# Optimization experiments

Measured on AMD Instinct MI355X. Metric: run time of the kernel, lower is better.

Reference implementation:

```python
import jax, jax.numpy as jnp
import numpy as np

N_USER = 50000
N_ITEM = 30000
NNZ = 500000  # user-item interactions; edges duplicated symmetrically -> E = 2*NNZ
EMB = 64
N_LAYERS = 2
N_FACTORS = 4
N_ITERATIONS = 2


def setup_inputs() -> dict:
    key = jax.random.key(0)
    k1, k2, k3, k4 = jax.random.split(key, 4)
    user_emb = jax.random.normal(k1, (N_USER, EMB), dtype=jnp.float32) * 0.1
    item_emb = jax.random.normal(k2, (N_ITEM, EMB), dtype=jnp.float32) * 0.1
    row = jax.random.randint(k3, (NNZ,), 0, N_USER, dtype=jnp.int32)
    col = jax.random.randint(k4, (NNZ,), 0, N_ITEM, dtype=jnp.int32) + N_USER
    # symmetric edge list exactly as the torch module builds it
    all_h_list = jnp.concatenate([row, col], axis=0)
    all_t_list = jnp.concatenate([col, row], axis=0)
    return {"user_emb": user_emb, "item_emb": item_emb,
            "all_h_list": all_h_list, "all_t_list": all_t_list}


def _dgcf_forward(user_emb, item_emb, all_h_list, all_t_list):
    n_user = user_emb.shape[0]
    ego = jnp.concatenate([user_emb, item_emb], axis=0)  # [N, D]
    N, D = ego.shape
    F = N_FACTORS
    d = D // F
    E = all_h_list.shape[0]
    dtype = ego.dtype

    all_embeddings = [ego]
    A = jnp.ones((E, F), dtype=dtype)  # A_values init

    for _layer in range(N_LAYERS):
        # torch.chunk along dim 1 == reshape [N, F, d]
        chunks = ego.reshape(N, F, d)
        tail_chunks = chunks[all_t_list]  # [E, F, d] gather of tail embeddings
        factor_emb = None
        for _t in range(N_ITERATIONS):
            # build_matrix, vectorized over the F factors
            normA = jax.nn.softmax(A, axis=1)                        # [E, F]
            dval = jax.ops.segment_sum(normA, all_h_list, num_segments=N)  # [N, F]
            dinv = 1.0 / jnp.sqrt(jnp.clip(dval, 1e-8))
            edge_weight = normA * dinv[all_h_list] * dinv[all_t_list]  # [E, F]
            # message passing per factor: gather tail, weight, scatter to head
            edge_val = tail_chunks * edge_weight[:, :, None]           # [E, F, d]
            factor_emb = jax.ops.segment_sum(edge_val, all_h_list, num_segments=N)  # [N, F, d]
            # dynamic routing update of A
            head = factor_emb[all_h_list]                              # [E, F, d]
            head = head / jnp.clip(jnp.linalg.norm(head, axis=-1, keepdims=True), 1e-12)
            tail = tail_chunks / jnp.clip(jnp.linalg.norm(tail_chunks, axis=-1, keepdims=True), 1e-12)
            A_iter = jnp.sum(head * jnp.tanh(tail), axis=-1)           # [E, F]
            A = A + A_iter
        ego = factor_emb.reshape(N, D)  # concat of factor chunks (last iteration)
        all_embeddings.append(ego)

    all_emb = jnp.mean(jnp.stack(all_embeddings, axis=1), axis=1)  # [N, D]
    return all_emb[:n_user], all_emb[n_user:]


def reference(user_emb, item_emb, all_h_list, all_t_list):
    return _dgcf_forward(user_emb, item_emb, all_h_list, all_t_list)
```

## Files before the change

kernel.cpp:

```cpp
#include <hip/hip_runtime.h>
#include <hip/hip_bf16.h>

#define N_USER 50000
#define N_ITEM 30000
#define NTOT   80000
#define EMB    64
#define FAC    4
#define EDGES  1000000
#define LOG4   1.3862943611198906f
#define NBUCK  512
#define BBLK   512
#define BCH    1954


__device__ inline float bf2f(unsigned short u) {
    return __uint_as_float(((unsigned int)u) << 16);
}
__device__ inline unsigned short f2bf(float f) {
    unsigned int x = __float_as_uint(f);
    x += 0x7FFFu + ((x >> 16) & 1u);
    return (unsigned short)(x >> 16);
}
__device__ inline float dot2(unsigned int a, unsigned int b) {
    float a0 = __uint_as_float(a << 16), a1 = __uint_as_float(a & 0xFFFF0000u);
    float b0 = __uint_as_float(b << 16), b1 = __uint_as_float(b & 0xFFFF0000u);
    return a0 * b0 + a1 * b1;
}
__device__ inline int bucket_of(int h) { return (int)(((unsigned)h * NBUCK) / (unsigned)NTOT); }
__device__ inline int bucket_lo(int k) { return (k * NTOT + NBUCK - 1) / NBUCK; }

__global__ void k_detect(const unsigned short* __restrict__ raw, int* __restrict__ flag) {
    __shared__ int s;
    if (threadIdx.x == 0) s = 0;
    __syncthreads();
    int c = 0;
    for (int i = threadIdx.x; i < 16384; i += 256) {
        unsigned short u = raw[i];
        if ((u & 0x7F80) == 0x7F80) c++;
    }
    atomicAdd(&s, c);
    __syncthreads();
    if (threadIdx.x == 0) *flag = (s > 0) ? 1 : 0;
}

__global__ void k_init(const void* __restrict__ ue, const void* __restrict__ ie,
                       const int* __restrict__ flag,
                       unsigned short* __restrict__ egoh,
                       unsigned short* __restrict__ tnh0) {
    int gid = blockIdx.x * blockDim.x + threadIdx.x;
    int wid = gid >> 6;
    int lane = threadIdx.x & 63;
    if (wid >= NTOT) return;
    int i = wid * 64 + lane;
    bool isf32 = (*flag != 0);
    float v;
    if (i < N_USER * EMB) {
        v = isf32 ? ((const float*)ue)[i]
                  : __bfloat162float(((const __hip_bfloat16*)ue)[i]);
    } else {
        int j = i - N_USER * EMB;
        v = isf32 ? ((const float*)ie)[j]
                  : __bfloat162float(((const __hip_bfloat16*)ie)[j]);
    }
    egoh[i] = f2bf(v);
    float ss = v * v;
    ss += __shfl_xor(ss, 1); ss += __shfl_xor(ss, 2);
    ss += __shfl_xor(ss, 4); ss += __shfl_xor(ss, 8);
    float rr = 1.0f / fmaxf(sqrtf(ss), 1e-12f);
    tnh0[i] = f2bf(tanhf(v * rr));
}

__global__ void k_bcnt(const int* __restrict__ hl, int* __restrict__ cnt) {
    __shared__ int hist[NBUCK];
    int b = blockIdx.x, tid = threadIdx.x;
    for (int i = tid; i < NBUCK; i += 256) hist[i] = 0;
    __syncthreads();
    int base = b * BCH, end = base + BCH; if (end > EDGES) end = EDGES;
    for (int e = base + tid; e < end; e += 256)
        atomicAdd(&hist[bucket_of(hl[e])], 1);
    __syncthreads();
    for (int i = tid; i < NBUCK; i += 256) cnt[b * NBUCK + i] = hist[i];
}

__global__ void k_btot(const int* __restrict__ cnt, int* __restrict__ boff) {
    __shared__ int sbuf[NBUCK];
    int k = threadIdx.x;
    int s = 0;
    for (int b = 0; b < BBLK; ++b) s += cnt[b * NBUCK + k];
    sbuf[k] = s;
    __syncthreads();
    int v = s;
    for (int st = 1; st < NBUCK; st <<= 1) {
        int t = (k >= st) ? sbuf[k - st] : 0;
        __syncthreads();
        sbuf[k] += t;
        __syncthreads();
    }
    boff[k] = sbuf[k] - v;
    if (k == NBUCK - 1) boff[NBUCK] = EDGES;
}

__global__ void k_bscan(const int* __restrict__ cnt, const int* __restrict__ boff,
                        int* __restrict__ gbase) {
    __shared__ int buf[BBLK];
    int k = blockIdx.x, tid = threadIdx.x;
    int v = cnt[tid * NBUCK + k];
    buf[tid] = v;
    __syncthreads();
    for (int s = 1; s < BBLK; s <<= 1) {
        int t = (tid >= s) ? buf[tid - s] : 0;
        __syncthreads();
        buf[tid] += t;
        __syncthreads();
    }
    gbase[tid * NBUCK + k] = boff[k] + buf[tid] - v;
}

__global__ void k_bscat(const int* __restrict__ hl, const int* __restrict__ tl,
                        const int* __restrict__ gbase, int* __restrict__ bt) {
    __shared__ int lg[NBUCK];
    int b = blockIdx.x, tid = threadIdx.x;
    for (int i = tid; i < NBUCK; i += 256) lg[i] = gbase[b * NBUCK + i];
    __syncthreads();
    int base = b * BCH, end = base + BCH; if (end > EDGES) end = EDGES;
    for (int e = base + tid; e < end; e += 256) {
        int h = hl[e];
        int k = bucket_of(h);
        int pos = atomicAdd(&lg[k], 1);
        bt[pos] = ((h - bucket_lo(k)) << 17) | tl[e];
    }
}

__global__ void k_bfin(const int* __restrict__ bt, const int* __restrict__ boff,
                       int* __restrict__ off, float* __restrict__ dvacc,
                       int* __restrict__ tlist, int* __restrict__ hlist) {
    __shared__ int ldeg[160];
    __shared__ int lcur[160];
    __shared__ int sbuf[256];
    int k = blockIdx.x, tid = threadIdx.x;
    int lo = bucket_lo(k), hi = bucket_lo(k + 1);
    int nn = hi - lo;
    for (int i = tid; i < nn; i += 256) ldeg[i] = 0;
    __syncthreads();
    int start = boff[k], end = boff[k + 1];
    for (int j = start + tid; j < end; j += 256)
        atomicAdd(&ldeg[bt[j] >> 17], 1);
    __syncthreads();
    int v = (tid < nn) ? ldeg[tid] : 0;
    sbuf[tid] = v;
    __syncthreads();
    for (int s = 1; s < 256; s <<= 1) {
        int t = (tid >= s) ? sbuf[tid - s] : 0;
        __syncthreads();
        sbuf[tid] += t;
        __syncthreads();
    }
    if (tid < nn) {
        int o = start + sbuf[tid] - v;
        off[lo + tid] = o;
        lcur[tid] = o;
        float d = 0.25f * (float)v;
        ((float4*)dvacc)[lo + tid] = make_float4(d, d, d, d);
    }
    if (k == 0 && tid == 0) off[NTOT] = EDGES;
    __syncthreads();
    for (int j = start + tid; j < end; j += 256) {
        int val = bt[j];
        int hrel = val >> 17;
        int t = val & 0x1FFFF;
        int pos = atomicAdd(&lcur[hrel], 1);
        tlist[pos] = t;
        hlist[pos] = lo + hrel;
    }
}

__global__ void k_scale(float* __restrict__ dvacc, float* __restrict__ dvinv,
                        const unsigned short* __restrict__ ego,
                        unsigned short* __restrict__ egoS) {
    int gid = blockIdx.x * blockDim.x + threadIdx.x;
    int wid = gid >> 6;
    int lane = threadIdx.x & 63;
    if (wid >= NTOT) return;
    int f = lane >> 4;
    float r = rsqrtf(fmaxf(dvacc[wid * 4 + f], 1e-8f));
    if ((lane & 15) == 0) dvinv[wid * 4 + f] = r;
    if (lane < 4) dvacc[wid * 4 + lane] = 0.f;
    int i = wid * 64 + lane;
    egoS[i] = f2bf(bf2f(ego[i]) * r);
}

__global__ void k_mp(const unsigned short* __restrict__ egoS, const float* __restrict__ P,
                     const float* __restrict__ dvinv, const int* __restrict__ off,
                     const int* __restrict__ tlist,
                     unsigned short* __restrict__ fach, float* __restrict__ rhn,
                     unsigned short* __restrict__ tnhOut,
                     int useP, int writeRhn, int writeTnh) {
    int gid = blockIdx.x * blockDim.x + threadIdx.x;
    int wid = gid >> 6;
    int lane = threadIdx.x & 63;
    if (wid >= NTOT) return;
    int c = lane & 15;
    int q = lane >> 4;
    int f = c >> 2;
    int beg = off[wid], end = off[wid + 1];
    float dvh = dvinv[wid * 4 + f];
    const uint2* eg2 = (const uint2*)egoS;

    float a0 = 0.f, a1 = 0.f, a2 = 0.f, a3 = 0.f;
    int nfull = (end - beg) >> 2;
    int j = beg + q;
    if (useP) {
#pragma unroll 2
        for (int g = 0; g < nfull; ++g, j += 4) {
            int t = tlist[j];
            float w = P[j * 4 + f];
            uint2 u = eg2[t * 16 + c];
            a0 += w * __uint_as_float(u.x << 16);
            a1 += w * __uint_as_float(u.x & 0xFFFF0000u);
            a2 += w * __uint_as_float(u.y << 16);
            a3 += w * __uint_as_float(u.y & 0xFFFF0000u);
        }
        if (j < end) {
            int t = tlist[j];
            float w = P[j * 4 + f];
            uint2 u = eg2[t * 16 + c];
            a0 += w * __uint_as_float(u.x << 16);
            a1 += w * __uint_as_float(u.x & 0xFFFF0000u);
            a2 += w * __uint_as_float(u.y << 16);
            a3 += w * __uint_as_float(u.y & 0xFFFF0000u);
        }
    } else {
#pragma unroll 2
        for (int g = 0; g < nfull; ++g, j += 4) {
            int t = tlist[j];
            uint2 u = eg2[t * 16 + c];
            a0 += __uint_as_float(u.x << 16);
            a1 += __uint_as_float(u.x & 0xFFFF0000u);
            a2 += __uint_as_float(u.y << 16);
            a3 += __uint_as_float(u.y & 0xFFFF0000u);
        }
        if (j < end) {
            int t = tlist[j];
            uint2 u = eg2[t * 16 + c];
            a0 += __uint_as_float(u.x << 16);
            a1 += __uint_as_float(u.x & 0xFFFF0000u);
            a2 += __uint_as_float(u.y << 16);
            a3 += __uint_as_float(u.y & 0xFFFF0000u);
        }
        a0 *= 0.25f; a1 *= 0.25f; a2 *= 0.25f; a3 *= 0.25f;
    }

    a0 += __shfl_xor(a0, 16); a1 += __shfl_xor(a1, 16);
    a2 += __shfl_xor(a2, 16); a3 += __shfl_xor(a3, 16);
    a0 += __shfl_xor(a0, 32); a1 += __shfl_xor(a1, 32);
    a2 += __shfl_xor(a2, 32); a3 += __shfl_xor(a3, 32);

    a0 *= dvh; a1 *= dvh; a2 *= dvh; a3 *= dvh;

    if (q == 0) {
        unsigned int p01 = (unsigned int)f2bf(a0) | ((unsigned int)f2bf(a1) << 16);
        unsigned int p23 = (unsigned int)f2bf(a2) | ((unsigned int)f2bf(a3) << 16);
        ((uint2*)fach)[wid * 16 + c] = make_uint2(p01, p23);
    }

    if (writeRhn || writeTnh) {
        float ss = a0 * a0 + a1 * a1 + a2 * a2 + a3 * a3;
        ss += __shfl_xor(ss, 1); ss += __shfl_xor(ss, 2);
        float rr = 1.0f / fmaxf(sqrtf(ss), 1e-12f);
        if (writeRhn && q == 0 && (c & 3) == 0) rhn[wid * 4 + f] = rr;
        if (writeTnh) {
            float t0 = tanhf(a0 * rr), t1 = tanhf(a1 * rr),
                  t2 = tanhf(a2 * rr), t3 = tanhf(a3 * rr);
            if (q == 0) {
                unsigned int p01 = (unsigned int)f2bf(t0) | ((unsigned int)f2bf(t1) << 16);
                unsigned int p23 = (unsigned int)f2bf(t2) | ((unsigned int)f2bf(t3) << 16);
                ((uint2*)tnhOut)[wid * 16 + c] = make_uint2(p01, p23);
            }
        }
    }
}

__global__ void k_upd(const unsigned short* __restrict__ fach,
                      const unsigned short* __restrict__ tnhh,
                      const float* __restrict__ rhn,
                      const int* __restrict__ hlist, const int* __restrict__ tlist,
                      float* __restrict__ P, float* __restrict__ dval, int first) {
    __shared__ int   s_h[256];
    __shared__ float s_p[256][4];
    int tid = threadIdx.x;
    int j = blockIdx.x * 256 + tid;
    int h = -1;
    if (j < EDGES) {
        h = hlist[j];
        int t = tlist[j];
        const uint4* frow = (const uint4*)(fach + (size_t)h * 64);
        const uint4* trow = (const uint4*)(tnhh + (size_t)t * 64);
        float d[4];
#pragma unroll
        for (int f = 0; f < 4; ++f) {
            uint4 a0 = frow[f * 2], a1 = frow[f * 2 + 1];
            uint4 b0 = trow[f * 2], b1 = trow[f * 2 + 1];
            d[f] = dot2(a0.x, b0.x) + dot2(a0.y, b0.y)
                 + dot2(a0.z, b0.z) + dot2(a0.w, b0.w)
                 + dot2(a1.x, b1.x) + dot2(a1.y, b1.y)
                 + dot2(a1.z, b1.z) + dot2(a1.w, b1.w);
        }
        float4 rh = ((const float4*)rhn)[h];
        float lx, ly, lz, lw;
        if (first) { lx = ly = lz = lw = -LOG4; }
        else {
            float4 p0 = ((const float4*)P)[j];
            lx = __logf(p0.x); ly = __logf(p0.y);
            lz = __logf(p0.z); lw = __logf(p0.w);
        }
        float y0 = lx + rh.x * d[0], y1 = ly + rh.y * d[1],
              y2 = lz + rh.z * d[2], y3 = lw + rh.w * d[3];
        float m = fmaxf(fmaxf(y0, y1), fmaxf(y2, y3));
        float e0 = __expf(y0 - m), e1 = __expf(y1 - m),
              e2 = __expf(y2 - m), e3 = __expf(y3 - m);
        float inv = 1.0f / (e0 + e1 + e2 + e3);
        float p0n = e0 * inv, p1n = e1 * inv, p2n = e2 * inv, p3n = e3 * inv;
        ((float4*)P)[j] = make_float4(p0n, p1n, p2n, p3n);
        s_p[tid][0] = p0n; s_p[tid][1] = p1n; s_p[tid][2] = p2n; s_p[tid][3] = p3n;
    }
    s_h[tid] = h;
    __syncthreads();
    if (h == -1) return;
    if (tid > 0 && s_h[tid - 1] == h) return;
    float a0 = 0.f, a1 = 0.f, a2 = 0.f, a3 = 0.f;
    int k = tid;
    while (k < 256 && s_h[k] == h) {
        a0 += s_p[k][0]; a1 += s_p[k][1]; a2 += s_p[k][2]; a3 += s_p[k][3];
        ++k;
    }
    float* dst = dval + (size_t)h * 4;
    if (tid == 0 || k == 256) {
        unsafeAtomicAdd(dst + 0, a0);
        unsafeAtomicAdd(dst + 1, a1);
        unsafeAtomicAdd(dst + 2, a2);
        unsafeAtomicAdd(dst + 3, a3);
    } else {
        ((float4*)dst)[0] = make_float4(a0, a1, a2, a3);
    }
}

__global__ void k_final(const void* __restrict__ ue, const void* __restrict__ ie,
                        const int* __restrict__ flag,
                        const unsigned short* __restrict__ f1,
                        const unsigned short* __restrict__ f3,
                        float* __restrict__ out) {
    int i = blockIdx.x * blockDim.x + threadIdx.x;
    if (i >= NTOT * EMB) return;
    bool isf32 = (*flag != 0);
    float v;
    if (i < N_USER * EMB) {
        v = isf32 ? ((const float*)ue)[i]
                  : __bfloat162float(((const __hip_bfloat16*)ue)[i]);
    } else {
        int j = i - N_USER * EMB;
        v = isf32 ? ((const float*)ie)[j]
                  : __bfloat162float(((const __hip_bfloat16*)ie)[j]);
    }
    out[i] = (v + bf2f(f1[i]) + bf2f(f3[i])) * (1.0f / 3.0f);
}

extern "C" void kernel_launch(void* const* d_in, const int* in_sizes, int n_in,
                              void* d_out, int out_size, void* d_ws, size_t ws_size,
                              hipStream_t stream) {
    const void* ue = d_in[0];
    const void* ie = d_in[1];
    const int* hl = (const int*)d_in[2];
    const int* tl = (const int*)d_in[3];
    float* out = (float*)d_out;

    float* ws    = (float*)d_ws;
    float* P     = ws;
    int*   bt    = (int*)(ws);
    int*   cnt   = (int*)(ws + 1000000);
    int*   gbase = (int*)(ws + 1262144);
    float* dvacc = ws + 4000000;
    float* dvinv = ws + 4320000;
    float* rhn   = ws + 4640000;
    unsigned short* bufW = (unsigned short*)(ws + 4960000);
    unsigned short* bufX = (unsigned short*)(ws + 7520000);
    unsigned short* bufY = (unsigned short*)(ws + 10080000);
    unsigned short* bufZ0 = (unsigned short*)(ws + 12640000);
    unsigned short* bufZ1 = (unsigned short*)(ws + 15200000);
    unsigned short* egoS = (unsigned short*)(ws + 17760000);
    int*   flag = (int*)(ws + 20320000);
    int*   boff = (int*)(ws + 20320016);
    int*   off  = (int*)(ws + 20400016);
    int*   tlist = (int*)(ws + 20480017);
    int*   hlist = (int*)(ws + 21480017);

    k_detect<<<1, 256, 0, stream>>>((const unsigned short*)ue, flag);
    k_init<<<20000, 256, 0, stream>>>(ue, ie, flag, bufW, bufZ0);

    k_bcnt<<<BBLK, 256, 0, stream>>>(hl, cnt);
    k_btot<<<1, NBUCK, 0, stream>>>(cnt, boff);
    k_bscan<<<NBUCK, BBLK, 0, stream>>>(cnt, boff, gbase);
    k_bscat<<<BBLK, 256, 0, stream>>>(hl, tl, gbase, bt);
    k_bfin<<<NBUCK, 256, 0, stream>>>(bt, boff, off, dvacc, tlist, hlist);

    k_scale<<<20000, 256, 0, stream>>>(dvacc, dvinv, bufW, egoS);
    k_mp<<<20000, 256, 0, stream>>>(egoS, P, dvinv, off, tlist, bufX, rhn, bufZ1,
                                    0, 1, 0);
    k_upd<<<3907, 256, 0, stream>>>(bufX, bufZ0, rhn, hlist, tlist, P, dvacc, 1);
    k_scale<<<20000, 256, 0, stream>>>(dvacc, dvinv, bufW, egoS);
    k_mp<<<20000, 256, 0, stream>>>(egoS, P, dvinv, off, tlist, bufY, rhn, bufZ1,
                                    1, 1, 1);
    k_upd<<<3907, 256, 0, stream>>>(bufY, bufZ0, rhn, hlist, tlist, P, dvacc, 0);
    k_scale<<<20000, 256, 0, stream>>>(dvacc, dvinv, bufY, egoS);
    k_mp<<<20000, 256, 0, stream>>>(egoS, P, dvinv, off, tlist, bufX, rhn, bufZ1,
                                    1, 1, 0);
    k_upd<<<3907, 256, 0, stream>>>(bufX, bufZ1, rhn, hlist, tlist, P, dvacc, 0);
    k_scale<<<20000, 256, 0, stream>>>(dvacc, dvinv, bufY, egoS);
    k_mp<<<20000, 256, 0, stream>>>(egoS, P, dvinv, off, tlist, bufW, rhn, bufZ1,
                                    1, 0, 0);
    k_final<<<20000, 256, 0, stream>>>(ue, ie, flag, bufY, bufW, out);
}
```

Baseline: 441.1 us.

## Fuse routing-update pass into the CSR message-passing kernel

Folds the per-edge routing/softmax update (previously a separate edge-parallel kernel reading the head-factor embedding, a norm buffer and an hlist array) into the node-wise CSR message-passing kernel. Each wavefront keeps its just-computed head factor and norm in registers, re-walks its neighbour list to compute dot products with tail tanh embeddings, updates P, and writes the degree sums directly without atomics. This removes a kernel launch, the hlist array, the rhn buffer and the atomic degree accumulation. In exchange, the second neighbour walk runs inside the lane-serial CSR loop with extra shuffles, and the per-edge P accesses become strided scalar loads.

Result: slower. 484.1 us (+9.7%).

```diff
diff --git a/kernel.cpp b/kernel.cpp
--- a/kernel.cpp
+++ b/kernel.cpp
@@ -20,11 +20,6 @@
     unsigned int x = __float_as_uint(f);
     x += 0x7FFFu + ((x >> 16) & 1u);
     return (unsigned short)(x >> 16);
-}
-__device__ inline float dot2(unsigned int a, unsigned int b) {
-    float a0 = __uint_as_float(a << 16), a1 = __uint_as_float(a & 0xFFFF0000u);
-    float b0 = __uint_as_float(b << 16), b1 = __uint_as_float(b & 0xFFFF0000u);
-    return a0 * b0 + a1 * b1;
 }
 __device__ inline int bucket_of(int h) { return (int)(((unsigned)h * NBUCK) / (unsigned)NTOT); }
 __device__ inline int bucket_lo(int k) { return (k * NTOT + NBUCK - 1) / NBUCK; }
@@ -133,7 +128,7 @@
 
 __global__ void k_bfin(const int* __restrict__ bt, const int* __restrict__ boff,
                        int* __restrict__ off, float* __restrict__ dvacc,
-                       int* __restrict__ tlist, int* __restrict__ hlist) {
+                       int* __restrict__ tlist) {
     __shared__ int ldeg[160];
     __shared__ int lcur[160];
     __shared__ int sbuf[256];
@@ -170,11 +165,10 @@
         int t = val & 0x1FFFF;
         int pos = atomicAdd(&lcur[hrel], 1);
         tlist[pos] = t;
-        hlist[pos] = lo + hrel;
-    }
-}
-
-__global__ void k_scale(float* __restrict__ dvacc, float* __restrict__ dvinv,
+    }
+}
+
+__global__ void k_scale(const float* __restrict__ dvacc, float* __restrict__ dvinv,
                         const unsigned short* __restrict__ ego,
                         unsigned short* __restrict__ egoS) {
     int gid = blockIdx.x * blockDim.x + threadIdx.x;
@@ -184,17 +178,18 @@
     int f = lane >> 4;
     float r = rsqrtf(fmaxf(dvacc[wid * 4 + f], 1e-8f));
     if ((lane & 15) == 0) dvinv[wid * 4 + f] = r;
-    if (lane < 4) dvacc[wid * 4 + lane] = 0.f;
     int i = wid * 64 + lane;
     egoS[i] = f2bf(bf2f(ego[i]) * r);
 }
 
-__global__ void k_mp(const unsigned short* __restrict__ egoS, const float* __restrict__ P,
+__global__ void k_mp(const unsigned short* __restrict__ egoS, float* __restrict__ P,
                      const float* __restrict__ dvinv, const int* __restrict__ off,
                      const int* __restrict__ tlist,
-                     unsigned short* __restrict__ fach, float* __restrict__ rhn,
+                     unsigned short* __restrict__ fach,
+                     const unsigned short* __restrict__ tnhIn,
                      unsigned short* __restrict__ tnhOut,
-                     int useP, int writeRhn, int writeTnh) {
+                     float* __restrict__ dvacc,
+                     int useP, int writeTnh, int doUpd, int first) {
     int gid = blockIdx.x * blockDim.x + threadIdx.x;
     int wid = gid >> 6;
     int lane = threadIdx.x & 63;
@@ -263,84 +258,62 @@
         ((uint2*)fach)[wid * 16 + c] = make_uint2(p01, p23);
     }
 
-    if (writeRhn || writeTnh) {
+    float rr = 0.f;
+    if (writeTnh || doUpd) {
         float ss = a0 * a0 + a1 * a1 + a2 * a2 + a3 * a3;
         ss += __shfl_xor(ss, 1); ss += __shfl_xor(ss, 2);
-        float rr = 1.0f / fmaxf(sqrtf(ss), 1e-12f);
-        if (writeRhn && q == 0 && (c & 3) == 0) rhn[wid * 4 + f] = rr;
-        if (writeTnh) {
-            float t0 = tanhf(a0 * rr), t1 = tanhf(a1 * rr),
-                  t2 = tanhf(a2 * rr), t3 = tanhf(a3 * rr);
-            if (q == 0) {
-                unsigned int p01 = (unsigned int)f2bf(t0) | ((unsigned int)f2bf(t1) << 16);
-                unsigned int p23 = (unsigned int)f2bf(t2) | ((unsigned int)f2bf(t3) << 16);
-                ((uint2*)tnhOut)[wid * 16 + c] = make_uint2(p01, p23);
-            }
-        }
-    }
-}
-
-__global__ void k_upd(const unsigned short* __restrict__ fach,
-                      const unsigned short* __restrict__ tnhh,
-                      const float* __restrict__ rhn,
-                      const int* __restrict__ hlist, const int* __restrict__ tlist,
-                      float* __restrict__ P, float* __restrict__ dval, int first) {
-    __shared__ int   s_h[256];
-    __shared__ float s_p[256][4];
-    int tid = threadIdx.x;
-    int j = blockIdx.x * 256 + tid;
-    int h = -1;
-    if (j < EDGES) {
-        h = hlist[j];
-        int t = tlist[j];
-        const uint4* frow = (const uint4*)(fach + (size_t)h * 64);
-        const uint4* trow = (const uint4*)(tnhh + (size_t)t * 64);
-        float d[4];
-#pragma unroll
-        for (int f = 0; f < 4; ++f) {
-            uint4 a0 = frow[f * 2], a1 = frow[f * 2 + 1];
-            uint4 b0 = trow[f * 2], b1 = trow[f * 2 + 1];
-            d[f] = dot2(a0.x, b0.x) + dot2(a0.y, b0.y)
-                 + dot2(a0.z, b0.z) + dot2(a0.w, b0.w)
-                 + dot2(a1.x, b1.x) + dot2(a1.y, b1.y)
-                 + dot2(a1.z, b1.z) + dot2(a1.w, b1.w);
-        }
-        float4 rh = ((const float4*)rhn)[h];
-        float lx, ly, lz, lw;
-        if (first) { lx = ly = lz = lw = -LOG4; }
-        else {
-            float4 p0 = ((const float4*)P)[j];
-            lx = __logf(p0.x); ly = __logf(p0.y);
-            lz = __logf(p0.z); lw = __logf(p0.w);
-        }
-        float y0 = lx + rh.x * d[0], y1 = ly + rh.y * d[1],
-              y2 = lz + rh.z * d[2], y3 = lw + rh.w * d[3];
-        float m = fmaxf(fmaxf(y0, y1), fmaxf(y2, y3));
-        float e0 = __expf(y0 - m), e1 = __expf(y1 - m),
-              e2 = __expf(y2 - m), e3 = __expf(y3 - m);
-        float inv = 1.0f / (e0 + e1 + e2 + e3);
-        float p0n = e0 * inv, p1n = e1 * inv, p2n = e2 * inv, p3n = e3 * inv;
-        ((float4*)P)[j] = make_float4(p0n, p1n, p2n, p3n);
-        s_p[tid][0] = p0n; s_p[tid][1] = p1n; s_p[tid][2] = p2n; s_p[tid][3] = p3n;
-    }
-    s_h[tid] = h;
-    __syncthreads();
-    if (h == -1) return;
-    if (tid > 0 && s_h[tid - 1] == h) return;
-    float a0 = 0.f, a1 = 0.f, a2 = 0.f, a3 = 0.f;
-    int k = tid;
-    while (k < 256 && s_h[k] == h) {
-        a0 += s_p[k][0]; a1 += s_p[k][1]; a2 += s_p[k][2]; a3 += s_p[k][3];
-        ++k;
-    }
-    float* dst = dval + (size_t)h * 4;
-    if (tid == 0 || k == 256) {
-        unsafeAtomicAdd(dst + 0, a0);
-        unsafeAtomicAdd(dst + 1, a1);
-        unsafeAtomicAdd(dst + 2, a2);
-        unsafeAtomicAdd(dst + 3, a3);
-    } else {
-        ((float4*)dst)[0] = make_float4(a0, a1, a2, a3);
+        rr = 1.0f / fmaxf(sqrtf(ss), 1e-12f);
+    }
+    if (writeTnh) {
+        float t0 = tanhf(a0 * rr), t1 = tanhf(a1 * rr),
+              t2 = tanhf(a2 * rr), t3 = tanhf(a3 * rr);
+        if (q == 0) {
+            unsigned int p01 = (unsigned int)f2bf(t0) | ((unsigned int)f2bf(t1) << 16);
+            unsigned int p23 = (unsigned int)f2bf(t2) | ((unsigned int)f2bf(t3) << 16);
+            ((uint2*)tnhOut)[wid * 16 + c] = make_uint2(p01, p23);
+        }
+    }
+
+    if (doUpd) {
+        const uint2* th2 = (const uint2*)tnhIn;
+        float dvf = 0.f;
+        int j2 = beg + q;
+        for (int g = 0; g < nfull; ++g, j2 += 4) {
+            int t = tlist[j2];
+            uint2 u = th2[t * 16 + c];
+            float pd = a0 * __uint_as_float(u.x << 16)
+                     + a1 * __uint_as_float(u.x & 0xFFFF0000u)
+                     + a2 * __uint_as_float(u.y << 16)
+                     + a3 * __uint_as_float(u.y & 0xFFFF0000u);
+            pd += __shfl_xor(pd, 1); pd += __shfl_xor(pd, 2);
+            float lp = first ? -LOG4 : __logf(P[j2 * 4 + f]);
+            float y = lp + rr * pd;
+            float m = fmaxf(y, __shfl_xor(y, 4)); m = fmaxf(m, __shfl_xor(m, 8));
+            float e = __expf(y - m);
+            float s = e + __shfl_xor(e, 4); s += __shfl_xor(s, 8);
+            float p = e / s;
+            if ((lane & 3) == 0) P[j2 * 4 + f] = p;
+            dvf += p;
+        }
+        if (j2 < end) {
+            int t = tlist[j2];
+            uint2 u = th2[t * 16 + c];
+            float pd = a0 * __uint_as_float(u.x << 16)
+                     + a1 * __uint_as_float(u.x & 0xFFFF0000u)
+                     + a2 * __uint_as_float(u.y << 16)
+                     + a3 * __uint_as_float(u.y & 0xFFFF0000u);
+            pd += __shfl_xor(pd, 1); pd += __shfl_xor(pd, 2);
+            float lp = first ? -LOG4 : __logf(P[j2 * 4 + f]);
+            float y = lp + rr * pd;
+            float m = fmaxf(y, __shfl_xor(y, 4)); m = fmaxf(m, __shfl_xor(m, 8));
+            float e = __expf(y - m);
+            float s = e + __shfl_xor(e, 4); s += __shfl_xor(s, 8);
+            float p = e / s;
+            if ((lane & 3) == 0) P[j2 * 4 + f] = p;
+            dvf += p;
+        }
+        dvf += __shfl_xor(dvf, 16); dvf += __shfl_xor(dvf, 32);
+        if ((lane & 51) == 0) dvacc[wid * 4 + f] = dvf;
     }
 }
 
@@ -380,7 +353,6 @@
     int*   gbase = (int*)(ws + 1262144);
     float* dvacc = ws + 4000000;
     float* dvinv = ws + 4320000;
-    float* rhn   = ws + 4640000;
     unsigned short* bufW = (unsigned short*)(ws + 4960000);
     unsigned short* bufX = (unsigned short*)(ws + 7520000);
     unsigned short* bufY = (unsigned short*)(ws + 10080000);
@@ -391,7 +363,6 @@
     int*   boff = (int*)(ws + 20320016);
     int*   off  = (int*)(ws + 20400016);
     int*   tlist = (int*)(ws + 20480017);
-    int*   hlist = (int*)(ws + 21480017);
 
     k_detect<<<1, 256, 0, stream>>>((const unsigned short*)ue, flag);
     k_init<<<20000, 256, 0, stream>>>(ue, ie, flag, bufW, bufZ0);
@@ -400,22 +371,19 @@
     k_btot<<<1, NBUCK, 0, stream>>>(cnt, boff);
     k_bscan<<<NBUCK, BBLK, 0, stream>>>(cnt, boff, gbase);
     k_bscat<<<BBLK, 256, 0, stream>>>(hl, tl, gbase, bt);
-    k_bfin<<<NBUCK, 256, 0, stream>>>(bt, boff, off, dvacc, tlist, hlist);
+    k_bfin<<<NBUCK, 256, 0, stream>>>(bt, boff, off, dvacc, tlist);
 
     k_scale<<<20000, 256, 0, stream>>>(dvacc, dvinv, bufW, egoS);
-    k_mp<<<20000, 256, 0, stream>>>(egoS, P, dvinv, off, tlist, bufX, rhn, bufZ1,
-                                    0, 1, 0);
-    k_upd<<<3907, 256, 0, stream>>>(bufX, bufZ0, rhn, hlist, tlist, P, dvacc, 1);
+    k_mp<<<20000, 256, 0, stream>>>(egoS, P, dvinv, off, tlist, bufX, bufZ0, bufZ1,
+                                    dvacc, 0, 0, 1, 1);
     k_scale<<<20000, 256, 0, stream>>>(dvacc, dvinv, bufW, egoS);
-    k_mp<<<20000, 256, 0, stream>>>(egoS, P, dvinv, off, tlist, bufY, rhn, bufZ1,
-                                    1, 1, 1);
-    k_upd<<<3907, 256, 0, stream>>>(bufY, bufZ0, rhn, hlist, tlist, P, dvacc, 0);
+    k_mp<<<20000, 256, 0, stream>>>(egoS, P, dvinv, off, tlist, bufY, bufZ0, bufZ1,
+                                    dvacc, 1, 1, 1, 0);
     k_scale<<<20000, 256, 0, stream>>>(dvacc, dvinv, bufY, egoS);
-    k_mp<<<20000, 256, 0, stream>>>(egoS, P, dvinv, off, tlist, bufX, rhn, bufZ1,
-                                    1, 1, 0);
-    k_upd<<<3907, 256, 0, stream>>>(bufX, bufZ1, rhn, hlist, tlist, P, dvacc, 0);
+    k_mp<<<20000, 256, 0, stream>>>(egoS, P, dvinv, off, tlist, bufX, bufZ1, bufZ1,
+                                    dvacc, 1, 0, 1, 0);
     k_scale<<<20000, 256, 0, stream>>>(dvacc, dvinv, bufY, egoS);
-    k_mp<<<20000, 256, 0, stream>>>(egoS, P, dvinv, off, tlist, bufW, rhn, bufZ1,
-                                    1, 0, 0);
+    k_mp<<<20000, 256, 0, stream>>>(egoS, P, dvinv, off, tlist, bufW, bufZ1, bufZ1,
+                                    dvacc, 1, 0, 0, 0);
     k_final<<<20000, 256, 0, stream>>>(ue, ie, flag, bufY, bufW, out);
 }
```
